# Performance work log

Hardware: AMD Instinct MI355X
Metric: run time of the kernel (lower is better)

## Reference

```python
import jax, jax.numpy as jnp
import numpy as np

B, S, D, E, K, H = 2, 1024, 1024, 8, 2, 2048
Z_COEF = 1e-4  # router_z_loss_coef


def setup_inputs() -> dict:
    key = jax.random.key(0)
    ks = jax.random.split(key, 9)
    std = 0.02
    return {
        "x": jax.random.normal(ks[0], (B, S, D), jnp.float32),
        "router_w": jax.random.normal(ks[1], (E, D), jnp.float32) * std,
        "router_bias": jnp.zeros((E,), jnp.float32),
        "gate_w": jax.random.normal(ks[2], (E, H, D), jnp.float32) * std,
        "up_w": jax.random.normal(ks[3], (E, H, D), jnp.float32) * std,
        "down_w": jax.random.normal(ks[4], (E, D, H), jnp.float32) * std,
        "sh_gate_w": jax.random.normal(ks[5], (H, D), jnp.float32) * std,
        "sh_up_w": jax.random.normal(ks[6], (H, D), jnp.float32) * std,
        "sh_down_w": jax.random.normal(ks[7], (D, H), jnp.float32) * std,
    }


def reference(x, router_w, router_bias, gate_w, up_w, down_w, sh_gate_w, sh_up_w, sh_down_w):
    b, s, d = x.shape
    flat = x.reshape(-1, d)                                   # [N, D]
    n_tokens = flat.shape[0]

    # ---- router ----
    logits = flat @ router_w.T                                # [N, E]
    biased = logits + jax.lax.stop_gradient(router_bias)      # bias is detached
    _, topk_idx = jax.lax.top_k(biased, K)                    # [N, K]
    topk_logits = jnp.take_along_axis(logits, topk_idx, axis=-1)
    topk_weights = jax.nn.softmax(topk_logits.astype(jnp.float32), axis=-1).astype(x.dtype)

    router_z = jax.nn.logsumexp(logits.astype(jnp.float32), axis=-1)
    router_z_loss = jnp.mean(router_z ** 2) * Z_COEF

    # ---- load-balance stats (detached in the original via no_grad) ----
    full_probs = jax.lax.stop_gradient(jax.nn.softmax(logits.astype(jnp.float32), axis=-1))
    p_i = full_probs.mean(axis=0)                             # [E]
    mask = jnp.zeros_like(full_probs).at[jnp.arange(n_tokens)[:, None], topk_idx].set(1.0)
    f_i = mask.mean(axis=0)                                   # [E]
    load_balance = jnp.sum(p_i * f_i) * E
    aux_loss = jnp.zeros((), x.dtype)                         # load_balancing == "aux_loss_free"

    # ---- routed experts ----
    # Identical math to gather(weights)[token] + SwiGLU einsum + scatter-add:
    # out[n] = sum_k w[n,k] * SwiGLU_{idx[n,k]}(x[n]), computed as E masked GEMMs
    # to avoid materializing [N*K, H, D] weight copies.
    routed = jnp.zeros_like(flat)
    for e in range(E):
        w_e = jnp.sum(topk_weights * (topk_idx == e), axis=-1)            # [N]
        h = jax.nn.silu(flat @ gate_w[e].T) * (flat @ up_w[e].T)          # [N, H]
        routed = routed + w_e[:, None] * (h @ down_w[e].T)                # [N, D]

    # ---- shared expert (num_shared_experts = 1) ----
    shared = (jax.nn.silu(flat @ sh_gate_w.T) * (flat @ sh_up_w.T)) @ sh_down_w.T

    hidden_states = (routed + shared).reshape(b, s, d)
    return hidden_states, aux_loss, router_z_loss, jax.lax.stop_gradient(load_balance)
```

## Files before the change

kernel.cpp:

```cpp
#include <hip/hip_runtime.h>

#define N_TOK 2048
#define DIM   1024
#define NE    8
#define HID   2048
#define A_SHARED 4096
#define OUT_HID (N_TOK * DIM)

typedef float v4f __attribute__((ext_vector_type(4)));
typedef short v8s __attribute__((ext_vector_type(8)));

#define OFF_XBF   0ull
#define OFF_H     4194304ull
#define OFF_GW    29360128ull
#define OFF_UW    67108864ull
#define OFF_DW    104857600ull
#define OFF_TOK   142606336ull
#define OFF_WL    (OFF_TOK + 24576ull)
#define OFF_IDX   (OFF_WL + 24576ull)
#define OFF_TW    (OFF_IDX + 16384ull)
#define OFF_STATS (OFF_TW + 16384ull)

struct Stats {
  int counts[NE];
  int fill[NE];
  int offs[NE + 2];
  float z2;
  float psum[NE];
};

__device__ __forceinline__ unsigned short f2bf(float f) {
  union { float f; unsigned u; } v; v.f = f;
  unsigned r = v.u + 0x7FFFu + ((v.u >> 16) & 1u);
  return (unsigned short)(r >> 16);
}
__device__ __forceinline__ unsigned pack2bf(float a, float b) {
  return (unsigned)f2bf(a) | ((unsigned)f2bf(b) << 16);
}

__device__ __forceinline__ void async_lds16(const void* g, void* l) {
  __builtin_amdgcn_global_load_lds(
      (const __attribute__((address_space(1))) void*)g,
      (__attribute__((address_space(3))) void*)l, 16, 0, 0);
}

__global__ __launch_bounds__(256) void cast_x_kernel(const float* __restrict__ x,
                                                     unsigned short* __restrict__ xbf) {
  int i = blockIdx.x * 256 + threadIdx.x;
  float4 v = ((const float4*)x)[i];
  uint2 o;
  o.x = pack2bf(v.x, v.y);
  o.y = pack2bf(v.z, v.w);
  ((uint2*)xbf)[i] = o;
}

#define VR 4718592
#define VE 4194304
__global__ __launch_bounds__(256) void cast_w_kernel(
    const float* __restrict__ g, const float* __restrict__ u, const float* __restrict__ dn,
    const float* __restrict__ shg, const float* __restrict__ shu, const float* __restrict__ shd,
    unsigned short* __restrict__ outw) {
  unsigned i = blockIdx.x * 256 + threadIdx.x;
  unsigned r = i / VR;
  unsigned j = i - r * VR;
  const float* eb = (r == 0) ? g : (r == 1) ? u : dn;
  const float* sb = (r == 0) ? shg : (r == 1) ? shu : shd;
  const float* src = (j < VE) ? eb + 4ull * j : sb + 4ull * (j - VE);
  float4 v = *(const float4*)src;
  uint2 o;
  o.x = pack2bf(v.x, v.y);
  o.y = pack2bf(v.z, v.w);
  ((uint2*)outw)[i] = o;
}

__global__ __launch_bounds__(256) void router_kernel(
    const float* __restrict__ x, const float* __restrict__ rw, const float* __restrict__ rb,
    int* __restrict__ idxbuf, float* __restrict__ twbuf, Stats* __restrict__ st) {
  int lane = threadIdx.x & 63;
  int wv = threadIdx.x >> 6;
  int n = blockIdx.x * 4 + wv;

  float acc[NE];
#pragma unroll
  for (int e = 0; e < NE; ++e) acc[e] = 0.f;

  const float4* x4 = (const float4*)(x + (size_t)n * DIM);
#pragma unroll
  for (int q = 0; q < 4; ++q) {
    float4 xv = x4[q * 64 + lane];
#pragma unroll
    for (int e = 0; e < NE; ++e) {
      const float4* w4 = (const float4*)(rw + (size_t)e * DIM);
      float4 wvv = w4[q * 64 + lane];
      acc[e] += xv.x * wvv.x + xv.y * wvv.y + xv.z * wvv.z + xv.w * wvv.w;
    }
  }
#pragma unroll
  for (int off = 32; off; off >>= 1) {
#pragma unroll
    for (int e = 0; e < NE; ++e) acc[e] += __shfl_xor(acc[e], off);
  }

  float mx = acc[0];
#pragma unroll
  for (int e = 1; e < NE; ++e) mx = fmaxf(mx, acc[e]);
  float pr[NE];
  float es = 0.f;
#pragma unroll
  for (int e = 0; e < NE; ++e) { pr[e] = __expf(acc[e] - mx); es += pr[e]; }
  float inv = 1.f / es;
#pragma unroll
  for (int e = 0; e < NE; ++e) pr[e] *= inv;
  float z = mx + __logf(es);

  float b0 = -1e30f; int i0 = 0;
#pragma unroll
  for (int e = 0; e < NE; ++e) {
    float bb = acc[e] + rb[e];
    if (bb > b0) { b0 = bb; i0 = e; }
  }
  float b1 = -1e30f; int i1 = 0;
#pragma unroll
  for (int e = 0; e < NE; ++e) {
    if (e == i0) continue;
    float bb = acc[e] + rb[e];
    if (bb > b1) { b1 = bb; i1 = e; }
  }
  float l0 = acc[i0], l1 = acc[i1];
  float m2 = fmaxf(l0, l1);
  float e0 = __expf(l0 - m2), e1 = __expf(l1 - m2);
  float den = 1.f / (e0 + e1);
  float w0 = e0 * den, w1 = e1 * den;

  __shared__ float redp[4][9];
  __shared__ int redc[4][8];
  if (lane == 0) {
    idxbuf[n * 2] = i0; idxbuf[n * 2 + 1] = i1;
    twbuf[n * 2] = w0;  twbuf[n * 2 + 1] = w1;
#pragma unroll
    for (int e = 0; e < NE; ++e) redp[wv][e] = pr[e];
    redp[wv][8] = z * z;
#pragma unroll
    for (int e = 0; e < NE; ++e) redc[wv][e] = (e == i0) + (e == i1);
  }
  __syncthreads();
  int t = threadIdx.x;
  if (t < 9) {
    float s = redp[0][t] + redp[1][t] + redp[2][t] + redp[3][t];
    if (t < 8) atomicAdd(&st->psum[t], s);
    else       atomicAdd(&st->z2, s);
  } else if (t >= 16 && t < 24) {
    int e = t - 16;
    atomicAdd(&st->counts[e], redc[0][e] + redc[1][e] + redc[2][e] + redc[3][e]);
  }
}

__global__ void scan_kernel(Stats* __restrict__ st, float* __restrict__ out) {
  if (threadIdx.x == 0 && blockIdx.x == 0) {
    int o = 0;
#pragma unroll
    for (int e = 0; e < NE; ++e) { st->offs[e] = o; o += st->counts[e]; }
    st->offs[NE] = o;
    st->offs[NE + 1] = o + N_TOK;
    float zl = st->z2 / (float)N_TOK * 1e-4f;
    float lb = 0.f;
#pragma unroll
    for (int e = 0; e < NE; ++e)
      lb += (st->psum[e] / (float)N_TOK) * ((float)st->counts[e] / (float)N_TOK);
    lb *= (float)NE;
    out[OUT_HID + 0] = 0.f;
    out[OUT_HID + 1] = zl;
    out[OUT_HID + 2] = lb;
  }
}

__global__ __launch_bounds__(256) void scatter_kernel(
    const int* __restrict__ idxbuf, const float* __restrict__ twbuf,
    Stats* __restrict__ st, int* __restrict__ tok, float* __restrict__ wl) {
  int n = blockIdx.x * 256 + threadIdx.x;
#pragma unroll
  for (int k = 0; k < 2; ++k) {
    int e = idxbuf[n * 2 + k];
    int pos = st->offs[e] + atomicAdd(&st->fill[e], 1);
    tok[pos] = n;
    wl[pos] = twbuf[n * 2 + k];
  }
  tok[A_SHARED + n] = n;
  wl[A_SHARED + n] = 1.f;
}


__global__ __launch_bounds__(256, 2) void gateup_kernel(
    const unsigned short* __restrict__ gwbf, const unsigned short* __restrict__ uwbf,
    const unsigned short* __restrict__ xbf, const int* __restrict__ tok,
    const Stats* __restrict__ st, unsigned short* __restrict__ hbuf) {
  int e = blockIdx.z;
  int seg0 = st->offs[e];
  int cnt = st->offs[e + 1] - seg0;
  int m0 = blockIdx.y * 128;
  if (m0 >= cnt) return;
  int n0 = blockIdx.x * 128;

  __shared__ alignas(16) unsigned short As[2][128 * 32];
  __shared__ alignas(16) unsigned short Bg[2][128 * 32];
  __shared__ alignas(16) unsigned short Bu[2][128 * 32];

  int tid = threadIdx.x, l = tid & 63, w = tid >> 6;
  int wr = w >> 1, wc = w & 1;

  int sj = l >> 3;
  int ss = (l & 7) ^ sj;
  int grow = 2 * sj + (ss >> 2);
  int gch = ss & 3;

  const unsigned short* ap[2];
  const unsigned short* gp[2];
  const unsigned short* up[2];
#pragma unroll
  for (int q = 0; q < 2; ++q) {
    int row = (w * 2 + q) * 16 + grow;
    int ar = m0 + row; if (ar > cnt - 1) ar = cnt - 1;
    ap[q] = xbf + (size_t)tok[seg0 + ar] * DIM + gch * 8;
    size_t wb = (size_t)e * HID * DIM + (size_t)(n0 + row) * DIM + gch * 8;
    gp[q] = gwbf + wb;
    up[q] = uwbf + wb;
  }

  int lh = (l & 15) >> 1;
  int lofs = lh * 64 + ((((l & 1) * 4 + (l >> 4)) ^ lh) * 8);

  v4f accg[4][4], accu[4][4];
#pragma unroll
  for (int mi = 0; mi < 4; ++mi)
#pragma unroll
    for (int ni = 0; ni < 4; ++ni) {
      accg[mi][ni] = (v4f){0.f, 0.f, 0.f, 0.f};
      accu[mi][ni] = (v4f){0.f, 0.f, 0.f, 0.f};
    }

#pragma unroll
  for (int q = 0; q < 2; ++q) {
    async_lds16(ap[q], &As[0][(w * 2 + q) * 512]);
    async_lds16(gp[q], &Bg[0][(w * 2 + q) * 512]);
    async_lds16(up[q], &Bu[0][(w * 2 + q) * 512]);
  }

  int pb = 0;
  for (int k0 = 0; k0 < DIM; k0 += 32, pb ^= 1) {
    __syncthreads();

    v8s af[4], bgf[4], buf_[4];
#pragma unroll
    for (int mi = 0; mi < 4; ++mi)
      af[mi] = *(const v8s*)&As[pb][(wr * 32 + mi * 8) * 64 + lofs];
#pragma unroll
    for (int ni = 0; ni < 4; ++ni) {
      bgf[ni]  = *(const v8s*)&Bg[pb][(wc * 32 + ni * 8) * 64 + lofs];
      buf_[ni] = *(const v8s*)&Bu[pb][(wc * 32 + ni * 8) * 64 + lofs];
    }

    if (k0 + 32 < DIM) {
      int nb = pb ^ 1;
      int kn = k0 + 32;
#pragma unroll
      for (int q = 0; q < 2; ++q) {
        async_lds16(ap[q] + kn, &As[nb][(w * 2 + q) * 512]);
        async_lds16(gp[q] + kn, &Bg[nb][(w * 2 + q) * 512]);
        async_lds16(up[q] + kn, &Bu[nb][(w * 2 + q) * 512]);
      }
    }

#pragma unroll
    for (int mi = 0; mi < 4; ++mi)
#pragma unroll
      for (int ni = 0; ni < 4; ++ni) {
        accg[mi][ni] = __builtin_amdgcn_mfma_f32_16x16x32_bf16(af[mi], bgf[ni], accg[mi][ni], 0, 0, 0);
        accu[mi][ni] = __builtin_amdgcn_mfma_f32_16x16x32_bf16(af[mi], buf_[ni], accu[mi][ni], 0, 0, 0);
      }
  }

  int col = l & 15, rq = (l >> 4) * 4;
#pragma unroll
  for (int mi = 0; mi < 4; ++mi) {
#pragma unroll
    for (int rr = 0; rr < 4; ++rr) {
      int rl = wr * 64 + mi * 16 + rq + rr;
      if (m0 + rl < cnt) {
        size_t rowb = (size_t)(seg0 + m0 + rl) * HID + n0 + wc * 64;
#pragma unroll
        for (int ni = 0; ni < 4; ++ni) {
          float g = accg[mi][ni][rr], u = accu[mi][ni][rr];
          hbuf[rowb + ni * 16 + col] = f2bf(g * u / (1.f + __expf(-g)));
        }
      }
    }
  }
}

__global__ __launch_bounds__(256, 2) void down_kernel(
    const unsigned short* __restrict__ dwbf, const unsigned short* __restrict__ hbuf,
    const int* __restrict__ tok, const float* __restrict__ wl,
    const Stats* __restrict__ st, float* __restrict__ out) {
  int e = blockIdx.z;
  int seg0 = st->offs[e];
  int cnt = st->offs[e + 1] - seg0;
  int m0 = blockIdx.y * 128;
  if (m0 >= cnt) return;
  int n0 = blockIdx.x * 128;

  __shared__ alignas(16) unsigned short As[2][128 * 32];
  __shared__ alignas(16) unsigned short Bs[2][128 * 32];

  int tid = threadIdx.x, l = tid & 63, w = tid >> 6;
  int wr = w >> 1, wc = w & 1;

  int sj = l >> 3;
  int ss = (l & 7) ^ sj;
  int grow = 2 * sj + (ss >> 2);
  int gch = ss & 3;

  const unsigned short* ap[2];
  const unsigned short* bp[2];
#pragma unroll
  for (int q = 0; q < 2; ++q) {
    int row = (w * 2 + q) * 16 + grow;
    int ar = m0 + row; if (ar > cnt - 1) ar = cnt - 1;
    ap[q] = hbuf + (size_t)(seg0 + ar) * HID + gch * 8;
    bp[q] = dwbf + (size_t)e * DIM * HID + (size_t)(n0 + row) * HID + gch * 8;
  }

  int lh = (l & 15) >> 1;
  int lofs = lh * 64 + ((((l & 1) * 4 + (l >> 4)) ^ lh) * 8);

  v4f acc[4][4];
#pragma unroll
  for (int mi = 0; mi < 4; ++mi)
#pragma unroll
    for (int ni = 0; ni < 4; ++ni) acc[mi][ni] = (v4f){0.f, 0.f, 0.f, 0.f};

#pragma unroll
  for (int q = 0; q < 2; ++q) {
    async_lds16(ap[q], &As[0][(w * 2 + q) * 512]);
    async_lds16(bp[q], &Bs[0][(w * 2 + q) * 512]);
  }

  int pb = 0;
  for (int k0 = 0; k0 < HID; k0 += 32, pb ^= 1) {
    __syncthreads();

    v8s af[4], bf[4];
#pragma unroll
    for (int mi = 0; mi < 4; ++mi)
      af[mi] = *(const v8s*)&As[pb][(wr * 32 + mi * 8) * 64 + lofs];
#pragma unroll
    for (int ni = 0; ni < 4; ++ni)
      bf[ni] = *(const v8s*)&Bs[pb][(wc * 32 + ni * 8) * 64 + lofs];

    if (k0 + 32 < HID) {
      int nb = pb ^ 1;
      int kn = k0 + 32;
#pragma unroll
      for (int q = 0; q < 2; ++q) {
        async_lds16(ap[q] + kn, &As[nb][(w * 2 + q) * 512]);
        async_lds16(bp[q] + kn, &Bs[nb][(w * 2 + q) * 512]);
      }
    }

#pragma unroll
    for (int mi = 0; mi < 4; ++mi)
#pragma unroll
      for (int ni = 0; ni < 4; ++ni)
        acc[mi][ni] = __builtin_amdgcn_mfma_f32_16x16x32_bf16(af[mi], bf[ni], acc[mi][ni], 0, 0, 0);
  }

  int col = l & 15, rq = (l >> 4) * 4;
#pragma unroll
  for (int mi = 0; mi < 4; ++mi) {
#pragma unroll
    for (int rr = 0; rr < 4; ++rr) {
      int rl = wr * 64 + mi * 16 + rq + rr;
      if (m0 + rl < cnt) {
        int t = tok[seg0 + m0 + rl];
        float wgt = wl[seg0 + m0 + rl];
        float* ob = out + (size_t)t * DIM + n0 + wc * 64;
#pragma unroll
        for (int ni = 0; ni < 4; ++ni)
          atomicAdd(ob + ni * 16 + col, acc[mi][ni][rr] * wgt);
      }
    }
  }
}

extern "C" void kernel_launch(void* const* d_in, const int* in_sizes, int n_in,
                              void* d_out, int out_size, void* d_ws, size_t ws_size,
                              hipStream_t stream) {
  const float* x   = (const float*)d_in[0];
  const float* rw  = (const float*)d_in[1];
  const float* rb  = (const float*)d_in[2];
  const float* gw  = (const float*)d_in[3];
  const float* uw  = (const float*)d_in[4];
  const float* dw  = (const float*)d_in[5];
  const float* shg = (const float*)d_in[6];
  const float* shu = (const float*)d_in[7];
  const float* shd = (const float*)d_in[8];
  float* out = (float*)d_out;
  char* ws = (char*)d_ws;

  unsigned short* xbf  = (unsigned short*)(ws + OFF_XBF);
  unsigned short* hbuf = (unsigned short*)(ws + OFF_H);
  unsigned short* gwbf = (unsigned short*)(ws + OFF_GW);
  unsigned short* uwbf = (unsigned short*)(ws + OFF_UW);
  unsigned short* dwbf = (unsigned short*)(ws + OFF_DW);
  int*   tok  = (int*)(ws + OFF_TOK);
  float* wl   = (float*)(ws + OFF_WL);
  int*   idxb = (int*)(ws + OFF_IDX);
  float* twb  = (float*)(ws + OFF_TW);
  Stats* st   = (Stats*)(ws + OFF_STATS);

  hipMemsetAsync(d_out, 0, (size_t)out_size * sizeof(float), stream);
  hipMemsetAsync(st, 0, sizeof(Stats), stream);

  cast_x_kernel<<<2048, 256, 0, stream>>>(x, xbf);
  cast_w_kernel<<<55296, 256, 0, stream>>>(gw, uw, dw, shg, shu, shd, gwbf);
  router_kernel<<<512, 256, 0, stream>>>(x, rw, rb, idxb, twb, st);
  scan_kernel<<<1, 64, 0, stream>>>(st, out);
  scatter_kernel<<<8, 256, 0, stream>>>(idxb, twb, st, tok, wl);
  gateup_kernel<<<dim3(16, 16, 9), 256, 0, stream>>>(gwbf, uwbf, xbf, tok, st, hbuf);
  down_kernel<<<dim3(8, 16, 9), 256, 0, stream>>>(dwbf, hbuf, tok, wl, st, out);
}
```

Baseline: 417.4 us.

## Fuse x cast into router, widen weight cast, shrink down tile, raise occupancy

The separate x-to-bf16 cast kernel is removed and the conversion is folded into the router kernel, which already reads x. The weight cast kernel now has each thread convert four float4s, cutting the grid by four. The down-projection GEMM tile is halved in M from 128 to 64 rows to launch more blocks and use fewer registers. Both GEMM kernels ask for 3 waves-per-SIMD occupancy instead of 2. Smaller down tiles mean more reloads of the down weights and more atomic traffic blocks, and the higher occupancy hint may force register spills in gateup.

```diff
diff --git a/kernel.cpp b/kernel.cpp
--- a/kernel.cpp
+++ b/kernel.cpp
@@ -44,38 +44,36 @@
       (__attribute__((address_space(3))) void*)l, 16, 0, 0);
 }
 
-__global__ __launch_bounds__(256) void cast_x_kernel(const float* __restrict__ x,
-                                                     unsigned short* __restrict__ xbf) {
-  int i = blockIdx.x * 256 + threadIdx.x;
-  float4 v = ((const float4*)x)[i];
-  uint2 o;
-  o.x = pack2bf(v.x, v.y);
-  o.y = pack2bf(v.z, v.w);
-  ((uint2*)xbf)[i] = o;
-}
-
 #define VR 4718592
 #define VE 4194304
 __global__ __launch_bounds__(256) void cast_w_kernel(
     const float* __restrict__ g, const float* __restrict__ u, const float* __restrict__ dn,
     const float* __restrict__ shg, const float* __restrict__ shu, const float* __restrict__ shd,
     unsigned short* __restrict__ outw) {
-  unsigned i = blockIdx.x * 256 + threadIdx.x;
-  unsigned r = i / VR;
-  unsigned j = i - r * VR;
+  unsigned b = blockIdx.x;
+  unsigned i0 = b * 1024;
+  unsigned r = i0 / VR;
+  unsigned j0 = i0 - r * VR;
   const float* eb = (r == 0) ? g : (r == 1) ? u : dn;
   const float* sb = (r == 0) ? shg : (r == 1) ? shu : shd;
-  const float* src = (j < VE) ? eb + 4ull * j : sb + 4ull * (j - VE);
-  float4 v = *(const float4*)src;
-  uint2 o;
-  o.x = pack2bf(v.x, v.y);
-  o.y = pack2bf(v.z, v.w);
-  ((uint2*)outw)[i] = o;
+  const float4* src4 = (const float4*)((j0 < VE) ? eb + 4ull * j0 : sb + 4ull * (j0 - VE));
+  uint2* dst = ((uint2*)outw) + i0;
+  float4 v[4];
+#pragma unroll
+  for (int k = 0; k < 4; ++k) v[k] = src4[threadIdx.x + k * 256];
+#pragma unroll
+  for (int k = 0; k < 4; ++k) {
+    uint2 o;
+    o.x = pack2bf(v[k].x, v[k].y);
+    o.y = pack2bf(v[k].z, v[k].w);
+    dst[threadIdx.x + k * 256] = o;
+  }
 }
 
 __global__ __launch_bounds__(256) void router_kernel(
     const float* __restrict__ x, const float* __restrict__ rw, const float* __restrict__ rb,
-    int* __restrict__ idxbuf, float* __restrict__ twbuf, Stats* __restrict__ st) {
+    int* __restrict__ idxbuf, float* __restrict__ twbuf, Stats* __restrict__ st,
+    unsigned short* __restrict__ xbf) {
   int lane = threadIdx.x & 63;
   int wv = threadIdx.x >> 6;
   int n = blockIdx.x * 4 + wv;
@@ -85,9 +83,14 @@
   for (int e = 0; e < NE; ++e) acc[e] = 0.f;
 
   const float4* x4 = (const float4*)(x + (size_t)n * DIM);
+  uint2* xb2 = (uint2*)(xbf + (size_t)n * DIM);
 #pragma unroll
   for (int q = 0; q < 4; ++q) {
     float4 xv = x4[q * 64 + lane];
+    uint2 o;
+    o.x = pack2bf(xv.x, xv.y);
+    o.y = pack2bf(xv.z, xv.w);
+    xb2[q * 64 + lane] = o;
 #pragma unroll
     for (int e = 0; e < NE; ++e) {
       const float4* w4 = (const float4*)(rw + (size_t)e * DIM);
@@ -190,7 +193,7 @@
 }
 
 
-__global__ __launch_bounds__(256, 2) void gateup_kernel(
+__global__ __launch_bounds__(256, 3) void gateup_kernel(
     const unsigned short* __restrict__ gwbf, const unsigned short* __restrict__ uwbf,
     const unsigned short* __restrict__ xbf, const int* __restrict__ tok,
     const Stats* __restrict__ st, unsigned short* __restrict__ hbuf) {
@@ -297,18 +300,18 @@
   }
 }
 
-__global__ __launch_bounds__(256, 2) void down_kernel(
+__global__ __launch_bounds__(256, 3) void down_kernel(
     const unsigned short* __restrict__ dwbf, const unsigned short* __restrict__ hbuf,
     const int* __restrict__ tok, const float* __restrict__ wl,
     const Stats* __restrict__ st, float* __restrict__ out) {
   int e = blockIdx.z;
   int seg0 = st->offs[e];
   int cnt = st->offs[e + 1] - seg0;
-  int m0 = blockIdx.y * 128;
+  int m0 = blockIdx.y * 64;
   if (m0 >= cnt) return;
   int n0 = blockIdx.x * 128;
 
-  __shared__ alignas(16) unsigned short As[2][128 * 32];
+  __shared__ alignas(16) unsigned short As[2][64 * 32];
   __shared__ alignas(16) unsigned short Bs[2][128 * 32];
 
   int tid = threadIdx.x, l = tid & 63, w = tid >> 6;
@@ -319,39 +322,38 @@
   int grow = 2 * sj + (ss >> 2);
   int gch = ss & 3;
 
-  const unsigned short* ap[2];
+  int rowA = w * 16 + grow;
+  int arA = m0 + rowA; if (arA > cnt - 1) arA = cnt - 1;
+  const unsigned short* ap = hbuf + (size_t)(seg0 + arA) * HID + gch * 8;
   const unsigned short* bp[2];
 #pragma unroll
   for (int q = 0; q < 2; ++q) {
     int row = (w * 2 + q) * 16 + grow;
-    int ar = m0 + row; if (ar > cnt - 1) ar = cnt - 1;
-    ap[q] = hbuf + (size_t)(seg0 + ar) * HID + gch * 8;
     bp[q] = dwbf + (size_t)e * DIM * HID + (size_t)(n0 + row) * HID + gch * 8;
   }
 
   int lh = (l & 15) >> 1;
   int lofs = lh * 64 + ((((l & 1) * 4 + (l >> 4)) ^ lh) * 8);
 
-  v4f acc[4][4];
-#pragma unroll
-  for (int mi = 0; mi < 4; ++mi)
+  v4f acc[2][4];
+#pragma unroll
+  for (int mi = 0; mi < 2; ++mi)
 #pragma unroll
     for (int ni = 0; ni < 4; ++ni) acc[mi][ni] = (v4f){0.f, 0.f, 0.f, 0.f};
 
-#pragma unroll
-  for (int q = 0; q < 2; ++q) {
-    async_lds16(ap[q], &As[0][(w * 2 + q) * 512]);
+  async_lds16(ap, &As[0][w * 512]);
+#pragma unroll
+  for (int q = 0; q < 2; ++q)
     async_lds16(bp[q], &Bs[0][(w * 2 + q) * 512]);
-  }
 
   int pb = 0;
   for (int k0 = 0; k0 < HID; k0 += 32, pb ^= 1) {
     __syncthreads();
 
-    v8s af[4], bf[4];
-#pragma unroll
-    for (int mi = 0; mi < 4; ++mi)
-      af[mi] = *(const v8s*)&As[pb][(wr * 32 + mi * 8) * 64 + lofs];
+    v8s af[2], bf[4];
+#pragma unroll
+    for (int mi = 0; mi < 2; ++mi)
+      af[mi] = *(const v8s*)&As[pb][(wr * 16 + mi * 8) * 64 + lofs];
 #pragma unroll
     for (int ni = 0; ni < 4; ++ni)
       bf[ni] = *(const v8s*)&Bs[pb][(wc * 32 + ni * 8) * 64 + lofs];
@@ -359,15 +361,14 @@
     if (k0 + 32 < HID) {
       int nb = pb ^ 1;
       int kn = k0 + 32;
-#pragma unroll
-      for (int q = 0; q < 2; ++q) {
-        async_lds16(ap[q] + kn, &As[nb][(w * 2 + q) * 512]);
+      async_lds16(ap + kn, &As[nb][w * 512]);
+#pragma unroll
+      for (int q = 0; q < 2; ++q)
         async_lds16(bp[q] + kn, &Bs[nb][(w * 2 + q) * 512]);
-      }
-    }
-
-#pragma unroll
-    for (int mi = 0; mi < 4; ++mi)
+    }
+
+#pragma unroll
+    for (int mi = 0; mi < 2; ++mi)
 #pragma unroll
       for (int ni = 0; ni < 4; ++ni)
         acc[mi][ni] = __builtin_amdgcn_mfma_f32_16x16x32_bf16(af[mi], bf[ni], acc[mi][ni], 0, 0, 0);
@@ -375,10 +376,10 @@
 
   int col = l & 15, rq = (l >> 4) * 4;
 #pragma unroll
-  for (int mi = 0; mi < 4; ++mi) {
+  for (int mi = 0; mi < 2; ++mi) {
 #pragma unroll
     for (int rr = 0; rr < 4; ++rr) {
-      int rl = wr * 64 + mi * 16 + rq + rr;
+      int rl = wr * 32 + mi * 16 + rq + rr;
       if (m0 + rl < cnt) {
         int t = tok[seg0 + m0 + rl];
         float wgt = wl[seg0 + m0 + rl];
@@ -420,11 +421,10 @@
   hipMemsetAsync(d_out, 0, (size_t)out_size * sizeof(float), stream);
   hipMemsetAsync(st, 0, sizeof(Stats), stream);
 
-  cast_x_kernel<<<2048, 256, 0, stream>>>(x, xbf);
-  cast_w_kernel<<<55296, 256, 0, stream>>>(gw, uw, dw, shg, shu, shd, gwbf);
-  router_kernel<<<512, 256, 0, stream>>>(x, rw, rb, idxb, twb, st);
+  cast_w_kernel<<<13824, 256, 0, stream>>>(gw, uw, dw, shg, shu, shd, gwbf);
+  router_kernel<<<512, 256, 0, stream>>>(x, rw, rb, idxb, twb, st, xbf);
   scan_kernel<<<1, 64, 0, stream>>>(st, out);
   scatter_kernel<<<8, 256, 0, stream>>>(idxb, twb, st, tok, wl);
   gateup_kernel<<<dim3(16, 16, 9), 256, 0, stream>>>(gwbf, uwbf, xbf, tok, st, hbuf);
-  down_kernel<<<dim3(8, 16, 9), 256, 0, stream>>>(dwbf, hbuf, tok, wl, st, out);
-}
+  down_kernel<<<dim3(8, 32, 9), 256, 0, stream>>>(dwbf, hbuf, tok, wl, st, out);
+}
```

Measured after the change: 852.4 us. +104.2%, slower.
